# Kernel tuning notes

Measured on AMD Instinct MI355X. Metric: run time of the kernel, lower is better.

Reference implementation:

```python
import jax, jax.numpy as jnp
import numpy as np

# constants matching CombinedLoss_dynamic(a=1.0, alpha=0.0257, source_intensity=1e5)
ALPHA = 0.0257
A = 1.0
NORM = 27353.34765625
SRC_INTENSITY = 100000.0 / NORM
FIRE_THRESHOLD = (1000.0 - 20.0) / NORM


def _laplace_kernel():
    # 7-point 3D Laplacian stencil, shape [1,1,3,3,3] (OIDHW)
    k = jnp.zeros((3, 3, 3), dtype=jnp.float32)
    k = k.at[1, 1, 1].set(-6.0)
    k = k.at[0, 1, 1].set(1.0).at[2, 1, 1].set(1.0)
    k = k.at[1, 0, 1].set(1.0).at[1, 2, 1].set(1.0)
    k = k.at[1, 1, 0].set(1.0).at[1, 1, 2].set(1.0)
    return k[None, None]


def _laplacian3d(x):
    # x: [B, 1, D, H, W]; groups = C = 1, zero padding 1 on each spatial dim
    kernel = _laplace_kernel().astype(x.dtype)
    return jax.lax.conv_general_dilated(
        x, kernel,
        window_strides=(1, 1, 1),
        padding=[(1, 1), (1, 1), (1, 1)],
        dimension_numbers=("NCDHW", "OIDHW", "NCDHW"),
    )


def setup_inputs() -> dict:
    key = jax.random.key(0)
    ks = jax.random.split(key, 4)
    B, C, D, H, W = 16, 1, 64, 128, 128
    shape = (B, C, D, H, W)
    return {
        "input": jax.random.normal(ks[0], shape, dtype=jnp.float32),
        "output": jax.random.normal(ks[1], shape, dtype=jnp.float32),
        "output_past": jax.random.normal(ks[2], shape, dtype=jnp.float32),
        "t": jnp.ones((B, C), dtype=jnp.float32),
        "t_past": jnp.zeros((B, C), dtype=jnp.float32),
        "target": jax.random.normal(ks[3], shape, dtype=jnp.float32),
    }


def reference(input, output, output_past, t, t_past, target):
    # temporal derivative: (out - out_past) / (t - t_past), t broadcast over DHW
    dt = (t - t_past)[:, :, None, None, None]  # [B,1,1,1,1]
    temporal_derivative = (output - output_past) / dt
    laplacian = _laplacian3d(input)
    source_term = jnp.where(input > FIRE_THRESHOLD,
                            jnp.float32(SRC_INTENSITY), jnp.float32(0.0))
    residual = temporal_derivative - ALPHA * laplacian - source_term
    p_loss = jnp.mean(residual * residual)
    mse = jnp.mean((output - target) ** 2)
    return mse + A * p_loss
```

## Files before the change

kernel.cpp:

```cpp
#include <hip/hip_runtime.h>

#define NORMC 27353.34765625f
__device__ __constant__ float kALPHA = 0.0257f;
#define SRC_INTENSITY (100000.0f / NORMC)
#define FIRE_THRESHOLD (980.0f / NORMC)

constexpr int Wd = 128, Hd = 128, Dd = 64, Bd = 16;
constexpr int HW = Hd * Wd;
constexpr long long NTOT = (long long)Bd * Dd * Hd * Wd;
constexpr int N4 = (int)(NTOT / 4);
constexpr int NBLOCKS = 2048;
constexpr int NTHREADS = 256;

__global__ __launch_bounds__(NTHREADS) void loss_main(
    const float* __restrict__ in,
    const float* __restrict__ outp_cur,
    const float* __restrict__ outp_past,
    const float* __restrict__ tvec,
    const float* __restrict__ tpvec,
    const float* __restrict__ tgt,
    float2* __restrict__ partial)
{
    const float alpha = kALPHA;
    float sp = 0.0f;
    float sm = 0.0f;

    for (int i4 = blockIdx.x * blockDim.x + threadIdx.x; i4 < N4;
         i4 += gridDim.x * blockDim.x) {
        const int idx = i4 << 2;
        const int x0 = idx & (Wd - 1);
        const int y  = (idx >> 7) & (Hd - 1);
        const int z  = (idx >> 14) & (Dd - 1);
        const int b  = idx >> 20;

        const float4 c = *(const float4*)(in + idx);
        float4 ym = make_float4(0.f, 0.f, 0.f, 0.f);
        float4 yp = make_float4(0.f, 0.f, 0.f, 0.f);
        float4 zm = make_float4(0.f, 0.f, 0.f, 0.f);
        float4 zp = make_float4(0.f, 0.f, 0.f, 0.f);
        if (y > 0)      ym = *(const float4*)(in + idx - Wd);
        if (y < Hd - 1) yp = *(const float4*)(in + idx + Wd);
        if (z > 0)      zm = *(const float4*)(in + idx - HW);
        if (z < Dd - 1) zp = *(const float4*)(in + idx + HW);
        const float xl = (x0 > 0)        ? in[idx - 1] : 0.0f;
        const float xr = (x0 < Wd - 4)   ? in[idx + 4] : 0.0f;

        const float lap0 = xl  + c.y + ym.x + yp.x + zm.x + zp.x - 6.0f * c.x;
        const float lap1 = c.x + c.z + ym.y + yp.y + zm.y + zp.y - 6.0f * c.y;
        const float lap2 = c.y + c.w + ym.z + yp.z + zm.z + zp.z - 6.0f * c.z;
        const float lap3 = c.z + xr  + ym.w + yp.w + zm.w + zp.w - 6.0f * c.w;

        const float dt = tvec[b] - tpvec[b];

        const float4 o  = *(const float4*)(outp_cur + idx);
        const float4 op = *(const float4*)(outp_past + idx);
        const float4 tg = *(const float4*)(tgt + idx);

        const float src0 = (c.x > FIRE_THRESHOLD) ? SRC_INTENSITY : 0.0f;
        const float src1 = (c.y > FIRE_THRESHOLD) ? SRC_INTENSITY : 0.0f;
        const float src2 = (c.z > FIRE_THRESHOLD) ? SRC_INTENSITY : 0.0f;
        const float src3 = (c.w > FIRE_THRESHOLD) ? SRC_INTENSITY : 0.0f;

        const float r0 = (o.x - op.x) / dt - alpha * lap0 - src0;
        const float r1 = (o.y - op.y) / dt - alpha * lap1 - src1;
        const float r2 = (o.z - op.z) / dt - alpha * lap2 - src2;
        const float r3 = (o.w - op.w) / dt - alpha * lap3 - src3;
        sp += r0 * r0 + r1 * r1 + r2 * r2 + r3 * r3;

        const float m0 = o.x - tg.x, m1 = o.y - tg.y;
        const float m2 = o.z - tg.z, m3 = o.w - tg.w;
        sm += m0 * m0 + m1 * m1 + m2 * m2 + m3 * m3;
    }

    #pragma unroll
    for (int off = 32; off > 0; off >>= 1) {
        sp += __shfl_down(sp, off);
        sm += __shfl_down(sm, off);
    }
    __shared__ float2 wsum[NTHREADS / 64];
    const int lane = threadIdx.x & 63;
    const int wid  = threadIdx.x >> 6;
    if (lane == 0) wsum[wid] = make_float2(sp, sm);
    __syncthreads();
    if (threadIdx.x == 0) {
        float ap = 0.0f, am = 0.0f;
        #pragma unroll
        for (int w = 0; w < NTHREADS / 64; ++w) { ap += wsum[w].x; am += wsum[w].y; }
        partial[blockIdx.x] = make_float2(ap, am);
    }
}

__global__ __launch_bounds__(256) void loss_reduce(
    const float2* __restrict__ partial, float* __restrict__ out)
{
    double sp = 0.0, sm = 0.0;
    for (int i = threadIdx.x; i < NBLOCKS; i += blockDim.x) {
        const float2 v = partial[i];
        sp += (double)v.x;
        sm += (double)v.y;
    }
    #pragma unroll
    for (int off = 32; off > 0; off >>= 1) {
        sp += __shfl_down(sp, off);
        sm += __shfl_down(sm, off);
    }
    __shared__ double wsp[4], wsm[4];
    const int lane = threadIdx.x & 63;
    const int wid  = threadIdx.x >> 6;
    if (lane == 0) { wsp[wid] = sp; wsm[wid] = sm; }
    __syncthreads();
    if (threadIdx.x == 0) {
        double tp = 0.0, tm = 0.0;
        #pragma unroll
        for (int w = 0; w < 4; ++w) { tp += wsp[w]; tm += wsm[w]; }
        const double invN = 1.0 / (double)NTOT;
        out[0] = (float)(tm * invN + tp * invN);
    }
}

extern "C" void kernel_launch(void* const* d_in, const int* in_sizes, int n_in,
                              void* d_out, int out_size, void* d_ws, size_t ws_size,
                              hipStream_t stream) {
    const float* in_   = (const float*)d_in[0];
    const float* out_  = (const float*)d_in[1];
    const float* outp_ = (const float*)d_in[2];
    const float* t_    = (const float*)d_in[3];
    const float* tp_   = (const float*)d_in[4];
    const float* tgt_  = (const float*)d_in[5];

    float2* partial = (float2*)d_ws;

    loss_main<<<NBLOCKS, NTHREADS, 0, stream>>>(in_, out_, outp_, t_, tp_, tgt_, partial);
    loss_reduce<<<1, 256, 0, stream>>>(partial, (float*)d_out);
}
```

Measured before the change: 49.56 us.

## March threads along z with register reuse of stencil planes

Each thread now walks 8 consecutive z planes at one (x4,y) position and rotates the previous, current and next planes through registers. This removes the redundant z-neighbour loads the grid-stride version made. Blocks are swizzled across the grid, and the streaming tensors (output, output_past, target) use nontemporal loads. The division by dt becomes one reciprocal multiply, and launch bounds ask for higher occupancy. Per-thread serial dependence grows and there are fewer independent memory streams per step, which may hurt latency hiding.

```diff
diff --git a/kernel.cpp b/kernel.cpp
--- a/kernel.cpp
+++ b/kernel.cpp
@@ -1,75 +1,96 @@
 #include <hip/hip_runtime.h>
 
+typedef float f4 __attribute__((ext_vector_type(4)));
+
 #define NORMC 27353.34765625f
-__device__ __constant__ float kALPHA = 0.0257f;
+#define ALPHA_C 0.0257f
 #define SRC_INTENSITY (100000.0f / NORMC)
 #define FIRE_THRESHOLD (980.0f / NORMC)
 
 constexpr int Wd = 128, Hd = 128, Dd = 64, Bd = 16;
-constexpr int HW = Hd * Wd;
+constexpr int W4 = Wd / 4;
+constexpr int HWc = Hd * Wd;
+constexpr int BZ = 8;
 constexpr long long NTOT = (long long)Bd * Dd * Hd * Wd;
-constexpr int N4 = (int)(NTOT / 4);
-constexpr int NBLOCKS = 2048;
-constexpr int NTHREADS = 256;
+constexpr int NBLK = 2048;
+constexpr int NTH = 256;
 
-__global__ __launch_bounds__(NTHREADS) void loss_main(
+__device__ __forceinline__ f4 ldg4(const float* p) {
+    return *(const f4*)p;
+}
+__device__ __forceinline__ f4 ldnt4(const float* p) {
+    return __builtin_nontemporal_load((const f4*)p);
+}
+
+__global__ __launch_bounds__(NTH, 8) void loss_main(
     const float* __restrict__ in,
-    const float* __restrict__ outp_cur,
-    const float* __restrict__ outp_past,
+    const float* __restrict__ outc,
+    const float* __restrict__ outp,
     const float* __restrict__ tvec,
     const float* __restrict__ tpvec,
     const float* __restrict__ tgt,
     float2* __restrict__ partial)
 {
-    const float alpha = kALPHA;
+    const int bid  = blockIdx.x;
+    const int sbid = (bid & 7) * (NBLK / 8) + (bid >> 3);
+    const int gtid = sbid * NTH + (int)threadIdx.x;
+
+    const int x4 = gtid & (W4 - 1);
+    const int y  = (gtid >> 5) & (Hd - 1);
+    const int zs = (gtid >> 12) & 7;
+    const int b  = gtid >> 15;
+    const int z0 = zs * BZ;
+
+    int idx = (((b << 6) + z0) << 14) + (y << 7) + (x4 << 2);
+
+    const float dt  = tvec[b] - tpvec[b];
+    const float rdt = 1.0f / dt;
+
+    const f4 zero4 = {0.f, 0.f, 0.f, 0.f};
+    const bool ym_ok = (y > 0), yp_ok = (y < Hd - 1);
+    const bool xl_ok = (x4 > 0), xr_ok = (x4 < W4 - 1);
+
+    f4 cm = (zs > 0) ? ldg4(in + idx - HWc) : zero4;
+    f4 cc = ldg4(in + idx);
+
     float sp = 0.0f;
     float sm = 0.0f;
 
-    for (int i4 = blockIdx.x * blockDim.x + threadIdx.x; i4 < N4;
-         i4 += gridDim.x * blockDim.x) {
-        const int idx = i4 << 2;
-        const int x0 = idx & (Wd - 1);
-        const int y  = (idx >> 7) & (Hd - 1);
-        const int z  = (idx >> 14) & (Dd - 1);
-        const int b  = idx >> 20;
+    #pragma unroll 2
+    for (int k = 0; k < BZ; ++k) {
+        const int z = z0 + k;
+        const f4 cn = (z < Dd - 1) ? ldg4(in + idx + HWc) : zero4;
+        const f4 ym = ym_ok ? ldg4(in + idx - Wd) : zero4;
+        const f4 yp = yp_ok ? ldg4(in + idx + Wd) : zero4;
+        const float xl = xl_ok ? in[idx - 1] : 0.0f;
+        const float xr = xr_ok ? in[idx + 4] : 0.0f;
+        const f4 o  = ldnt4(outc + idx);
+        const f4 op = ldnt4(outp + idx);
+        const f4 tg = ldnt4(tgt  + idx);
 
-        const float4 c = *(const float4*)(in + idx);
-        float4 ym = make_float4(0.f, 0.f, 0.f, 0.f);
-        float4 yp = make_float4(0.f, 0.f, 0.f, 0.f);
-        float4 zm = make_float4(0.f, 0.f, 0.f, 0.f);
-        float4 zp = make_float4(0.f, 0.f, 0.f, 0.f);
-        if (y > 0)      ym = *(const float4*)(in + idx - Wd);
-        if (y < Hd - 1) yp = *(const float4*)(in + idx + Wd);
-        if (z > 0)      zm = *(const float4*)(in + idx - HW);
-        if (z < Dd - 1) zp = *(const float4*)(in + idx + HW);
-        const float xl = (x0 > 0)        ? in[idx - 1] : 0.0f;
-        const float xr = (x0 < Wd - 4)   ? in[idx + 4] : 0.0f;
+        const float lap0 = xl   + cc.y + ym.x + yp.x + cm.x + cn.x - 6.0f * cc.x;
+        const float lap1 = cc.x + cc.z + ym.y + yp.y + cm.y + cn.y - 6.0f * cc.y;
+        const float lap2 = cc.y + cc.w + ym.z + yp.z + cm.z + cn.z - 6.0f * cc.z;
+        const float lap3 = cc.z + xr   + ym.w + yp.w + cm.w + cn.w - 6.0f * cc.w;
 
-        const float lap0 = xl  + c.y + ym.x + yp.x + zm.x + zp.x - 6.0f * c.x;
-        const float lap1 = c.x + c.z + ym.y + yp.y + zm.y + zp.y - 6.0f * c.y;
-        const float lap2 = c.y + c.w + ym.z + yp.z + zm.z + zp.z - 6.0f * c.z;
-        const float lap3 = c.z + xr  + ym.w + yp.w + zm.w + zp.w - 6.0f * c.w;
+        const float src0 = (cc.x > FIRE_THRESHOLD) ? SRC_INTENSITY : 0.0f;
+        const float src1 = (cc.y > FIRE_THRESHOLD) ? SRC_INTENSITY : 0.0f;
+        const float src2 = (cc.z > FIRE_THRESHOLD) ? SRC_INTENSITY : 0.0f;
+        const float src3 = (cc.w > FIRE_THRESHOLD) ? SRC_INTENSITY : 0.0f;
 
-        const float dt = tvec[b] - tpvec[b];
-
-        const float4 o  = *(const float4*)(outp_cur + idx);
-        const float4 op = *(const float4*)(outp_past + idx);
-        const float4 tg = *(const float4*)(tgt + idx);
-
-        const float src0 = (c.x > FIRE_THRESHOLD) ? SRC_INTENSITY : 0.0f;
-        const float src1 = (c.y > FIRE_THRESHOLD) ? SRC_INTENSITY : 0.0f;
-        const float src2 = (c.z > FIRE_THRESHOLD) ? SRC_INTENSITY : 0.0f;
-        const float src3 = (c.w > FIRE_THRESHOLD) ? SRC_INTENSITY : 0.0f;
-
-        const float r0 = (o.x - op.x) / dt - alpha * lap0 - src0;
-        const float r1 = (o.y - op.y) / dt - alpha * lap1 - src1;
-        const float r2 = (o.z - op.z) / dt - alpha * lap2 - src2;
-        const float r3 = (o.w - op.w) / dt - alpha * lap3 - src3;
+        const float r0 = (o.x - op.x) * rdt - ALPHA_C * lap0 - src0;
+        const float r1 = (o.y - op.y) * rdt - ALPHA_C * lap1 - src1;
+        const float r2 = (o.z - op.z) * rdt - ALPHA_C * lap2 - src2;
+        const float r3 = (o.w - op.w) * rdt - ALPHA_C * lap3 - src3;
         sp += r0 * r0 + r1 * r1 + r2 * r2 + r3 * r3;
 
         const float m0 = o.x - tg.x, m1 = o.y - tg.y;
         const float m2 = o.z - tg.z, m3 = o.w - tg.w;
         sm += m0 * m0 + m1 * m1 + m2 * m2 + m3 * m3;
+
+        cm = cc;
+        cc = cn;
+        idx += HWc;
     }
 
     #pragma unroll
@@ -77,7 +98,7 @@
         sp += __shfl_down(sp, off);
         sm += __shfl_down(sm, off);
     }
-    __shared__ float2 wsum[NTHREADS / 64];
+    __shared__ float2 wsum[NTH / 64];
     const int lane = threadIdx.x & 63;
     const int wid  = threadIdx.x >> 6;
     if (lane == 0) wsum[wid] = make_float2(sp, sm);
@@ -85,7 +106,7 @@
     if (threadIdx.x == 0) {
         float ap = 0.0f, am = 0.0f;
         #pragma unroll
-        for (int w = 0; w < NTHREADS / 64; ++w) { ap += wsum[w].x; am += wsum[w].y; }
+        for (int w = 0; w < NTH / 64; ++w) { ap += wsum[w].x; am += wsum[w].y; }
         partial[blockIdx.x] = make_float2(ap, am);
     }
 }
@@ -94,7 +115,7 @@
     const float2* __restrict__ partial, float* __restrict__ out)
 {
     double sp = 0.0, sm = 0.0;
-    for (int i = threadIdx.x; i < NBLOCKS; i += blockDim.x) {
+    for (int i = threadIdx.x; i < NBLK; i += blockDim.x) {
         const float2 v = partial[i];
         sp += (double)v.x;
         sm += (double)v.y;
@@ -130,6 +151,6 @@
 
     float2* partial = (float2*)d_ws;
 
-    loss_main<<<NBLOCKS, NTHREADS, 0, stream>>>(in_, out_, outp_, t_, tp_, tgt_, partial);
+    loss_main<<<NBLK, NTH, 0, stream>>>(in_, out_, outp_, t_, tp_, tgt_, partial);
     loss_reduce<<<1, 256, 0, stream>>>(partial, (float*)d_out);
 }
```

Measured after the change: 62.89 us. 26.9% more time.
